# Optimization experiments

Measured on AMD Instinct MI355X. Metric: run time of the kernel, lower is better.

Reference implementation:

```python
import jax, jax.numpy as jnp
import numpy as np

C_IN = 256
RED = 8
C_QK = C_IN // RED  # 32


def setup_inputs() -> dict:
    key = jax.random.key(0)
    ks = jax.random.split(key, 8)
    B, C, H, W = 4, C_IN, 64, 64
    x = jax.random.normal(ks[0], (B, C, H, W), dtype=jnp.float32)
    # 1x1 conv weights stored as (out_ch, in_ch); biases (out_ch,)
    s = 1.0 / np.sqrt(C)
    wq = jax.random.uniform(ks[1], (C_QK, C), minval=-s, maxval=s, dtype=jnp.float32)
    bq = jax.random.uniform(ks[2], (C_QK,), minval=-s, maxval=s, dtype=jnp.float32)
    wk = jax.random.uniform(ks[3], (C_QK, C), minval=-s, maxval=s, dtype=jnp.float32)
    bk = jax.random.uniform(ks[4], (C_QK,), minval=-s, maxval=s, dtype=jnp.float32)
    wv = jax.random.uniform(ks[5], (C, C), minval=-s, maxval=s, dtype=jnp.float32)
    bv = jax.random.uniform(ks[6], (C,), minval=-s, maxval=s, dtype=jnp.float32)
    # nn.Parameter(torch.zeros(1)) -> use small nonzero so gradients flow in tests
    gamma = jnp.full((1,), 0.5, dtype=jnp.float32)
    return {"x": x, "wq": wq, "bq": bq, "wk": wk, "bk": bk,
            "wv": wv, "bv": bv, "gamma": gamma}


def reference(x, wq, bq, wk, bk, wv, bv, gamma):
    B, C, H, W = x.shape
    N = H * W
    xf = x.reshape(B, C, N)                                  # (B,C,N)
    # 1x1 convs == per-pixel linear projections over channels
    q = jnp.einsum('dc,bcn->bdn', wq, xf) + bq[None, :, None]  # (B,Cqk,N)
    k = jnp.einsum('dc,bcn->bdn', wk, xf) + bk[None, :, None]  # (B,Cqk,N)
    v = jnp.einsum('oc,bcn->bon', wv, xf) + bv[None, :, None]  # (B,C,N)
    # attention[b,i,j] = <q[:,i], k[:,j]> ; softmax over j (no scaling, as in source)
    scores = jnp.einsum('bdi,bdj->bij', q, k)                 # (B,N,N)
    attn = jax.nn.softmax(scores, axis=-1)
    # out[b,c,i] = sum_j v[b,c,j] * attn[b,i,j]
    out = jnp.einsum('bcj,bij->bci', v, attn).reshape(B, C, H, W)
    return gamma * out + x
```

## Files before the change

kernel.cpp:

```cpp
#include <hip/hip_runtime.h>
#include <hip/hip_bf16.h>


#define NB     4
#define CC     256
#define CQK    32
#define NPIX   4096
#define NCHUNK 4
#define CHUNK  (NPIX / NCHUNK)
#define NT     (CHUNK / 64)

typedef float floatx4 __attribute__((ext_vector_type(4)));
typedef short shortx4 __attribute__((ext_vector_type(4)));
typedef short shortx8 __attribute__((ext_vector_type(8)));

__device__ __forceinline__ short f2bf(float f) {
  unsigned u = __float_as_uint(f);
  u += 0x7fffu + ((u >> 16) & 1u);
  return (short)(u >> 16);
}
__device__ __forceinline__ float bf2f(unsigned short u) {
  return __uint_as_float((unsigned)u << 16);
}
__device__ __forceinline__ unsigned pk2bf(float a, float b) {
  union { __hip_bfloat162 h; unsigned u; } cv;
  cv.h = __float22bfloat162_rn(make_float2(a, b));
  return cv.u;
}
__device__ __forceinline__ void gload16(const void* g, void* l) {
  __builtin_amdgcn_global_load_lds(
      (const __attribute__((address_space(1))) void*)g,
      (__attribute__((address_space(3))) void*)l, 16, 0, 0);
}

__global__ __launch_bounds__(256) void projx_kernel(
    const float* __restrict__ x,
    const float* __restrict__ wq, const float* __restrict__ bq,
    const float* __restrict__ wk, const float* __restrict__ bk,
    const float* __restrict__ wv, const float* __restrict__ bv,
    short* __restrict__ Qb, short* __restrict__ Kb, short* __restrict__ Vb)
{
  __shared__ short T[16 * 256];
  __shared__ short SQK[16 * 72];

  const int gid = blockIdx.x;
  const int b = gid >> 8, n0 = (gid & 255) * 16;
  const int t = threadIdx.x, lane = t & 63, w = t >> 6;
  const int lo = lane & 15, hi = lane >> 4;

  {
    const int nq = (t & 3) * 4;
    const int cl = t >> 2;
#pragma unroll
    for (int rr = 0; rr < 4; rr++) {
      const int c = rr * 64 + cl;
      const floatx4 v = *(const floatx4*)(
          x + ((size_t)(b * CC + c)) * NPIX + n0 + nq);
#pragma unroll
      for (int i = 0; i < 4; i++) {
        const int n = nq + i;
        T[n * 256 + rr * 64 + (cl ^ ((n & 7) << 3))] = f2bf(v[i]);
      }
    }
  }
  __syncthreads();

  const float* wrow[5];
#pragma unroll
  for (int rt = 0; rt < 5; rt++) {
    const int o = w * 80 + rt * 16 + lo;
    wrow[rt] = (o < 32) ? (wq + (size_t)o * CC)
             : (o < 64) ? (wk + (size_t)(o - 32) * CC)
                        : (wv + (size_t)(o - 64) * CC);
  }

  floatx4 acc[5];
#pragma unroll
  for (int r = 0; r < 5; r++) acc[r] = (floatx4){0.f, 0.f, 0.f, 0.f};

#pragma unroll
  for (int c0 = 0; c0 < CC; c0 += 32) {
    const int c = c0 + hi * 8;
    const shortx8 bf = *(const shortx8*)
        &T[lo * 256 + (c & 192) + ((c & 63) ^ ((lo & 7) << 3))];
#pragma unroll
    for (int rt = 0; rt < 5; rt++) {
      const float* ap = wrow[rt] + c0 + hi * 8;
      floatx4 a0 = *(const floatx4*)ap;
      floatx4 a1 = *(const floatx4*)(ap + 4);
      if (w == 0 && rt < 2) {
        a0 *= 1.44269504088896f; a1 *= 1.44269504088896f;
      }
      union { shortx8 s; unsigned u[4]; } au;
      au.u[0] = pk2bf(a0[0], a0[1]);
      au.u[1] = pk2bf(a0[2], a0[3]);
      au.u[2] = pk2bf(a1[0], a1[1]);
      au.u[3] = pk2bf(a1[2], a1[3]);
      acc[rt] = __builtin_amdgcn_mfma_f32_16x16x32_bf16(au.s, bf, acc[rt], 0, 0, 0);
    }
  }
  __syncthreads();

#pragma unroll
  for (int rt = 0; rt < 5; rt++) {
#pragma unroll
    for (int j = 0; j < 4; j++) {
      const int o = w * 80 + rt * 16 + hi * 4 + j;
      const float bs = (o < 32) ? bq[o] * 1.44269504088896f
                     : (o < 64) ? bk[o - 32] : bv[o - 64];
      const short hv = f2bf(acc[rt][j] + bs);
      if (o < 64) SQK[lo * 72 + o] = hv;
      else        Vb[((size_t)(b * CC + (o - 64))) * NPIX + n0 + lo] = hv;
    }
  }
  __syncthreads();

  if (t < 128) {
    const int isK = t >> 6;
    const int flat = (t & 63) * 8;
    const int n = flat >> 5, o = flat & 31;
    const shortx8 d = *(const shortx8*)&SQK[n * 72 + isK * 32 + o];
    short* base = isK ? Kb : Qb;
    *(shortx8*)(base + ((size_t)(b * NPIX + n0 + n)) * CQK + o) = d;
  }
}

__global__ __launch_bounds__(256, 2) void attn_kernel(
    const short* __restrict__ Qb, const short* __restrict__ Kb,
    const short* __restrict__ Vb,
    short* __restrict__ Opart, float* __restrict__ Lpart)
{
  __shared__ short Vl[2][16384];
  __shared__ short Kl[2][2048];
  __shared__ short Pl[4][1024];

  const int bc = blockIdx.x & 15, qt = blockIdx.x >> 4;
  const int b = bc & 3, ch = bc >> 2;
  const int q0 = qt * 128, kv0 = ch * CHUNK;
  const int tid = threadIdx.x, lane = tid & 63, w = tid >> 6;
  const int lo = lane & 15, hi = lane >> 4;

  const short* Kc = Kb + ((size_t)(b * NPIX + kv0)) * CQK;
  const short* Vc = Vb + (size_t)b * CC * NPIX + kv0;

  shortx8 qf[2];
#pragma unroll
  for (int qs = 0; qs < 2; qs++)
    qf[qs] = *(const shortx8*)(
        Qb + ((size_t)(b * NPIX + q0 + w * 32 + qs * 16 + lo)) * CQK + hi * 8);

  const int cV = w * 64 + (lane >> 3);
  const int pcV = lane & 7;
  const int kvK = w * 16 + (lane >> 2);
  const int lcK = (lane & 3) ^ ((kvK >> 1) & 3);

  floatx4 oacc[2][16];
#pragma unroll
  for (int qs = 0; qs < 2; qs++)
#pragma unroll
    for (int i = 0; i < 16; i++) oacc[qs][i] = (floatx4){0.f, 0.f, 0.f, 0.f};
  float l[2] = {0.f, 0.f};
  const floatx4 zero4 = (floatx4){0.f, 0.f, 0.f, 0.f};

#pragma unroll
  for (int i = 0; i < 8; i++) {
    const int c = cV + i * 8;
    gload16(Vc + (size_t)c * NPIX + (pcV ^ (c & 7)) * 8, &Vl[0][w * 4096 + i * 512]);
  }
  gload16(Kc + (size_t)kvK * CQK + lcK * 8, &Kl[0][w * 512]);
  __syncthreads();

  for (int t = 0; t < NT; t++) {
    const int buf = t & 1;

    if (t + 1 < NT) {
      const int j0n = (t + 1) * 64;
#pragma unroll
      for (int i = 0; i < 8; i++) {
        const int c = cV + i * 8;
        gload16(Vc + (size_t)c * NPIX + j0n + (pcV ^ (c & 7)) * 8,
                &Vl[buf ^ 1][w * 4096 + i * 512]);
      }
      gload16(Kc + (size_t)(j0n + kvK) * CQK + lcK * 8, &Kl[buf ^ 1][w * 512]);
    }

    floatx4 s[2][4];
#pragma unroll
    for (int ct = 0; ct < 4; ct++) {
      const int kv = ct * 16 + lo;
      const shortx8 kf = *(const shortx8*)
          &Kl[buf][kv * 32 + ((hi * 8) ^ (((kv >> 1) & 3) << 3))];
      s[0][ct] = __builtin_amdgcn_mfma_f32_16x16x32_bf16(kf, qf[0], zero4, 0, 0, 0);
      s[1][ct] = __builtin_amdgcn_mfma_f32_16x16x32_bf16(kf, qf[1], zero4, 0, 0, 0);
    }

    shortx8 pb[2][2];
#pragma unroll
    for (int qs = 0; qs < 2; qs++) {
      float rs = 0.f;
#pragma unroll
      for (int ct = 0; ct < 4; ct++) {
        const float p0 = exp2f(s[qs][ct][0]), p1 = exp2f(s[qs][ct][1]);
        const float p2 = exp2f(s[qs][ct][2]), p3 = exp2f(s[qs][ct][3]);
        rs += (p0 + p1) + (p2 + p3);
        uint2 u;
        u.x = pk2bf(p0, p1);
        u.y = pk2bf(p2, p3);
        *(uint2*)&Pl[w][lo * 64 + ((ct * 16 + hi * 4) ^ ((lo & 7) << 3))] = u;
      }
#pragma unroll
      for (int h = 0; h < 2; h++)
        pb[qs][h] = *(const shortx8*)
            &Pl[w][lo * 64 + ((h * 32 + hi * 8) ^ ((lo & 7) << 3))];
      rs += __shfl_xor(rs, 16);
      rs += __shfl_xor(rs, 32);
      l[qs] += rs;
    }

    __builtin_amdgcn_s_setprio(1);
#pragma unroll
    for (int ctv = 0; ctv < 16; ctv++) {
      const int c = ctv * 16 + lo;
      const int swz = (c & 7) << 3;
      const shortx8 va0 = *(const shortx8*)&Vl[buf][c * 64 + ((hi * 8) ^ swz)];
      const shortx8 va1 = *(const shortx8*)&Vl[buf][c * 64 + ((32 + hi * 8) ^ swz)];
      oacc[0][ctv] = __builtin_amdgcn_mfma_f32_16x16x32_bf16(va0, pb[0][0], oacc[0][ctv], 0, 0, 0);
      oacc[0][ctv] = __builtin_amdgcn_mfma_f32_16x16x32_bf16(va1, pb[0][1], oacc[0][ctv], 0, 0, 0);
      oacc[1][ctv] = __builtin_amdgcn_mfma_f32_16x16x32_bf16(va0, pb[1][0], oacc[1][ctv], 0, 0, 0);
      oacc[1][ctv] = __builtin_amdgcn_mfma_f32_16x16x32_bf16(va1, pb[1][1], oacc[1][ctv], 0, 0, 0);
    }
    __builtin_amdgcn_s_setprio(0);

    __syncthreads();
  }

  if (hi == 0) {
    Lpart[(size_t)bc * NPIX + q0 + w * 32 + lo] = l[0];
    Lpart[(size_t)bc * NPIX + q0 + w * 32 + 16 + lo] = l[1];
  }
#pragma unroll
  for (int qs = 0; qs < 2; qs++) {
    const int n = q0 + w * 32 + qs * 16 + lo;
#pragma unroll
    for (int ctv = 0; ctv < 16; ctv++)
#pragma unroll
      for (int j = 0; j < 4; j++) {
        const int c = ctv * 16 + hi * 4 + j;
        Opart[((size_t)bc * CC + c) * NPIX + n] = f2bf(oacc[qs][ctv][j]);
      }
  }
}

__global__ __launch_bounds__(256) void combine_kernel(
    const short* __restrict__ Opart, const float* __restrict__ Lpart,
    const float* __restrict__ x, const float* __restrict__ gamma,
    float* __restrict__ out)
{
  __shared__ float linv[256];
  const int gid = blockIdx.x;
  const int b = gid >> 8;
  const int c0 = ((gid >> 4) & 15) * 16;
  const int n0 = (gid & 15) * 256;
  const int t = threadIdx.x;

  if (t < 64) {
    const int n = n0 + t * 4;
    floatx4 sum = (floatx4){0.f, 0.f, 0.f, 0.f};
#pragma unroll
    for (int k = 0; k < NCHUNK; k++)
      sum += *(const floatx4*)(Lpart + (size_t)(k * NB + b) * NPIX + n);
#pragma unroll
    for (int i = 0; i < 4; i++) linv[t * 4 + i] = 1.0f / sum[i];
  }
  __syncthreads();

  const float g = gamma[0];
  const int il = t & 31, cw = t >> 5;
  const int n = n0 + il * 8;
  float li[8];
#pragma unroll
  for (int j = 0; j < 8; j++) li[j] = linv[il * 8 + j];

#pragma unroll
  for (int i = 0; i < 2; i++) {
    const int c = c0 + cw * 2 + i;
    float acc[8];
#pragma unroll
    for (int j = 0; j < 8; j++) acc[j] = 0.f;
#pragma unroll
    for (int k = 0; k < NCHUNK; k++) {
      const shortx8 o = *(const shortx8*)(
          Opart + ((size_t)((k * NB + b) * CC + c)) * NPIX + n);
#pragma unroll
      for (int j = 0; j < 8; j++) acc[j] += bf2f((unsigned short)o[j]);
    }
    const size_t idx = ((size_t)(b * CC + c)) * NPIX + n;
    const floatx4 x0 = *(const floatx4*)(x + idx);
    const floatx4 x1 = *(const floatx4*)(x + idx + 4);
    floatx4 r0, r1;
#pragma unroll
    for (int j = 0; j < 4; j++) {
      r0[j] = g * (acc[j] * li[j]) + x0[j];
      r1[j] = g * (acc[j + 4] * li[j + 4]) + x1[j];
    }
    *(floatx4*)(out + idx) = r0;
    *(floatx4*)(out + idx + 4) = r1;
  }
}

extern "C" void kernel_launch(void* const* d_in, const int* in_sizes, int n_in,
                              void* d_out, int out_size, void* d_ws, size_t ws_size,
                              hipStream_t stream) {
  const float* x     = (const float*)d_in[0];
  const float* wq    = (const float*)d_in[1];
  const float* bq    = (const float*)d_in[2];
  const float* wk    = (const float*)d_in[3];
  const float* bk    = (const float*)d_in[4];
  const float* wv    = (const float*)d_in[5];
  const float* bv    = (const float*)d_in[6];
  const float* gamma = (const float*)d_in[7];
  float* out = (float*)d_out;

  char* p = (char*)d_ws;
  short* Qb    = (short*)p; p += (size_t)NB * NPIX * CQK * 2;
  short* Kb    = (short*)p; p += (size_t)NB * NPIX * CQK * 2;
  short* Vb    = (short*)p; p += (size_t)NB * CC * NPIX * 2;
  short* Opart = (short*)p; p += (size_t)(NCHUNK * NB) * CC * NPIX * 2;
  float* Lpart = (float*)p; p += (size_t)(NCHUNK * NB) * NPIX * 4;

  projx_kernel<<<dim3(1024), dim3(256), 0, stream>>>(x, wq, bq, wk, bk, wv, bv, Qb, Kb, Vb);
  attn_kernel<<<dim3(512), dim3(256), 0, stream>>>(Qb, Kb, Vb, Opart, Lpart);
  combine_kernel<<<dim3(1024), dim3(256), 0, stream>>>(Opart, Lpart, x, gamma, out);
}
```

Before: 182.3 us.

## Pre-convert projection weights to bf16 and widen projection tiles to 32 pixels

Adds a small prep kernel that converts the Q/K/V weights to bf16 once per call, folding the log2(e) scale into the Q rows. The projection kernel then loads bf16 weights directly instead of converting fp32 weights inside every block. It also processes 32 pixels per block with 512 threads, halving the grid and reusing each weight load across two pixel groups. Separately, it removes the s_setprio bracketing around the PV MFMA loop in the attention kernel, which is an unrelated scheduling tweak. The cost is one extra kernel launch.

```diff
diff --git a/kernel.cpp b/kernel.cpp
--- a/kernel.cpp
+++ b/kernel.cpp
@@ -33,46 +33,57 @@
       (__attribute__((address_space(3))) void*)l, 16, 0, 0);
 }
 
-__global__ __launch_bounds__(256) void projx_kernel(
-    const float* __restrict__ x,
-    const float* __restrict__ wq, const float* __restrict__ bq,
-    const float* __restrict__ wk, const float* __restrict__ bk,
-    const float* __restrict__ wv, const float* __restrict__ bv,
+__global__ __launch_bounds__(256) void prep_kernel(
+    const float* __restrict__ wq, const float* __restrict__ wk,
+    const float* __restrict__ wv, short* __restrict__ Wall)
+{
+  const int e = (blockIdx.x * 256 + threadIdx.x) * 4;
+  const int o = e >> 8, c = e & 255;
+  const float* src = (o < 32) ? (wq + (size_t)o * CC + c)
+                   : (o < 64) ? (wk + (size_t)(o - 32) * CC + c)
+                              : (wv + (size_t)(o - 64) * CC + c);
+  const float scale = (o < 32) ? 1.44269504088896f : 1.0f;
+  const floatx4 v = *(const floatx4*)src;
+  shortx4 r;
+#pragma unroll
+  for (int i = 0; i < 4; i++) r[i] = f2bf(v[i] * scale);
+  *(shortx4*)(Wall + e) = r;
+}
+
+__global__ __launch_bounds__(512) void projx_kernel(
+    const float* __restrict__ x, const short* __restrict__ Wall,
+    const float* __restrict__ bq, const float* __restrict__ bk,
+    const float* __restrict__ bv,
     short* __restrict__ Qb, short* __restrict__ Kb, short* __restrict__ Vb)
 {
-  __shared__ short T[16 * 256];
-  __shared__ short SQK[16 * 72];
+  __shared__ short T[32 * 256];
+  __shared__ short SQK[32 * 72];
 
   const int gid = blockIdx.x;
-  const int b = gid >> 8, n0 = (gid & 255) * 16;
+  const int b = gid >> 7, n0 = (gid & 127) * 32;
   const int t = threadIdx.x, lane = t & 63, w = t >> 6;
   const int lo = lane & 15, hi = lane >> 4;
 
   {
-    const int nq = (t & 3) * 4;
-    const int cl = t >> 2;
-#pragma unroll
-    for (int rr = 0; rr < 4; rr++) {
-      const int c = rr * 64 + cl;
+    const int cl = t >> 3;
+    const int ln = t & 7;
+#pragma unroll
+    for (int p = 0; p < 4; p++) {
+      const int c = p * 64 + cl;
       const floatx4 v = *(const floatx4*)(
-          x + ((size_t)(b * CC + c)) * NPIX + n0 + nq);
+          x + ((size_t)(b * CC + c)) * NPIX + n0 + ln * 4);
 #pragma unroll
       for (int i = 0; i < 4; i++) {
-        const int n = nq + i;
-        T[n * 256 + rr * 64 + (cl ^ ((n & 7) << 3))] = f2bf(v[i]);
+        const int n = ln * 4 + i;
+        T[n * 256 + (c & 192) + ((c & 63) ^ ((n & 7) << 3))] = f2bf(v[i]);
       }
     }
   }
   __syncthreads();
 
-  const float* wrow[5];
-#pragma unroll
-  for (int rt = 0; rt < 5; rt++) {
-    const int o = w * 80 + rt * 16 + lo;
-    wrow[rt] = (o < 32) ? (wq + (size_t)o * CC)
-             : (o < 64) ? (wk + (size_t)(o - 32) * CC)
-                        : (wv + (size_t)(o - 64) * CC);
-  }
+  const int wn = w & 1, wo = w >> 1;
+  const int nn = wn * 16 + lo;
+  const short* arow = Wall + (size_t)(wo * 80 + lo) * CC + hi * 8;
 
   floatx4 acc[5];
 #pragma unroll
@@ -82,46 +93,35 @@
   for (int c0 = 0; c0 < CC; c0 += 32) {
     const int c = c0 + hi * 8;
     const shortx8 bf = *(const shortx8*)
-        &T[lo * 256 + (c & 192) + ((c & 63) ^ ((lo & 7) << 3))];
+        &T[nn * 256 + (c & 192) + ((c & 63) ^ ((nn & 7) << 3))];
 #pragma unroll
     for (int rt = 0; rt < 5; rt++) {
-      const float* ap = wrow[rt] + c0 + hi * 8;
-      floatx4 a0 = *(const floatx4*)ap;
-      floatx4 a1 = *(const floatx4*)(ap + 4);
-      if (w == 0 && rt < 2) {
-        a0 *= 1.44269504088896f; a1 *= 1.44269504088896f;
-      }
-      union { shortx8 s; unsigned u[4]; } au;
-      au.u[0] = pk2bf(a0[0], a0[1]);
-      au.u[1] = pk2bf(a0[2], a0[3]);
-      au.u[2] = pk2bf(a1[0], a1[1]);
-      au.u[3] = pk2bf(a1[2], a1[3]);
-      acc[rt] = __builtin_amdgcn_mfma_f32_16x16x32_bf16(au.s, bf, acc[rt], 0, 0, 0);
-    }
-  }
-  __syncthreads();
+      const shortx8 a = *(const shortx8*)(arow + (size_t)rt * 16 * CC + c0);
+      acc[rt] = __builtin_amdgcn_mfma_f32_16x16x32_bf16(a, bf, acc[rt], 0, 0, 0);
+    }
+  }
 
 #pragma unroll
   for (int rt = 0; rt < 5; rt++) {
 #pragma unroll
     for (int j = 0; j < 4; j++) {
-      const int o = w * 80 + rt * 16 + hi * 4 + j;
+      const int o = wo * 80 + rt * 16 + hi * 4 + j;
       const float bs = (o < 32) ? bq[o] * 1.44269504088896f
                      : (o < 64) ? bk[o - 32] : bv[o - 64];
       const short hv = f2bf(acc[rt][j] + bs);
-      if (o < 64) SQK[lo * 72 + o] = hv;
-      else        Vb[((size_t)(b * CC + (o - 64))) * NPIX + n0 + lo] = hv;
+      if (o < 64) SQK[nn * 72 + o] = hv;
+      else        Vb[((size_t)(b * CC + (o - 64))) * NPIX + n0 + nn] = hv;
     }
   }
   __syncthreads();
 
-  if (t < 128) {
-    const int isK = t >> 6;
-    const int flat = (t & 63) * 8;
-    const int n = flat >> 5, o = flat & 31;
-    const shortx8 d = *(const shortx8*)&SQK[n * 72 + isK * 32 + o];
+  if (t < 256) {
+    const int isK = t >> 7;
+    const int r = t & 127;
+    const int n = r >> 2, oseg = (r & 3) * 8;
+    const shortx8 d = *(const shortx8*)&SQK[n * 72 + isK * 32 + oseg];
     short* base = isK ? Kb : Qb;
-    *(shortx8*)(base + ((size_t)(b * NPIX + n0 + n)) * CQK + o) = d;
+    *(shortx8*)(base + ((size_t)(b * NPIX + n0 + n)) * CQK + oseg) = d;
   }
 }
 
@@ -217,7 +217,6 @@
       l[qs] += rs;
     }
 
-    __builtin_amdgcn_s_setprio(1);
 #pragma unroll
     for (int ctv = 0; ctv < 16; ctv++) {
       const int c = ctv * 16 + lo;
@@ -229,7 +228,6 @@
       oacc[1][ctv] = __builtin_amdgcn_mfma_f32_16x16x32_bf16(va0, pb[1][0], oacc[1][ctv], 0, 0, 0);
       oacc[1][ctv] = __builtin_amdgcn_mfma_f32_16x16x32_bf16(va1, pb[1][1], oacc[1][ctv], 0, 0, 0);
     }
-    __builtin_amdgcn_s_setprio(0);
 
     __syncthreads();
   }
@@ -322,13 +320,15 @@
   float* out = (float*)d_out;
 
   char* p = (char*)d_ws;
+  short* Wall  = (short*)p; p += (size_t)320 * CC * 2;
   short* Qb    = (short*)p; p += (size_t)NB * NPIX * CQK * 2;
   short* Kb    = (short*)p; p += (size_t)NB * NPIX * CQK * 2;
   short* Vb    = (short*)p; p += (size_t)NB * CC * NPIX * 2;
   short* Opart = (short*)p; p += (size_t)(NCHUNK * NB) * CC * NPIX * 2;
   float* Lpart = (float*)p; p += (size_t)(NCHUNK * NB) * NPIX * 4;
 
-  projx_kernel<<<dim3(1024), dim3(256), 0, stream>>>(x, wq, bq, wk, bk, wv, bv, Qb, Kb, Vb);
+  prep_kernel<<<dim3(80), dim3(256), 0, stream>>>(wq, wk, wv, Wall);
+  projx_kernel<<<dim3(512), dim3(512), 0, stream>>>(x, Wall, bq, bk, bv, Qb, Kb, Vb);
   attn_kernel<<<dim3(512), dim3(256), 0, stream>>>(Qb, Kb, Vb, Opart, Lpart);
   combine_kernel<<<dim3(1024), dim3(256), 0, stream>>>(Opart, Lpart, x, gamma, out);
 }
```

Result: faster. 162.0 us (-11.2%).
